# Performance work log

Measured on AMD Instinct MI355X. Metric: run time of the kernel, lower is better.

Reference implementation:

```python
import jax, jax.numpy as jnp
import numpy as np

B, L, D, H, FF = 2, 2048, 2048, 16, 8192
DH = D // H
NEG = -1e9


def setup_inputs() -> dict:
    key = jax.random.key(0)
    ks = jax.random.split(key, 9)
    x = jax.random.normal(ks[0], (B, L, D), dtype=jnp.float32)
    # additive causal mask, broadcastable to [B, H, L, L]
    causal = jnp.triu(jnp.full((L, L), NEG, dtype=jnp.float32), k=1)
    mask = causal[None, None, :, :]
    s = 1.0 / np.sqrt(D)
    Wq = jax.random.normal(ks[1], (D, D), dtype=jnp.float32) * s
    Wk = jax.random.normal(ks[2], (D, D), dtype=jnp.float32) * s
    Wv = jax.random.normal(ks[3], (D, D), dtype=jnp.float32) * s
    Wo = jax.random.normal(ks[4], (D, D), dtype=jnp.float32) * s
    W_up = jax.random.normal(ks[5], (FF, D), dtype=jnp.float32) * s
    b_up = jnp.zeros((FF,), dtype=jnp.float32)
    W_down = jax.random.normal(ks[6], (D, FF), dtype=jnp.float32) * (1.0 / np.sqrt(FF))
    return {"x": x, "mask": mask, "Wq": Wq, "Wk": Wk, "Wv": Wv, "Wo": Wo,
            "W_up": W_up, "b_up": b_up, "W_down": W_down}


def reference(x, mask, Wq, Wk, Wv, Wo, W_up, b_up, W_down):
    b, l, d = x.shape
    # projections (torch Linear: y = x @ W.T); reshape to [B, H, L, DH]
    q = (x @ Wq.T).reshape(b, l, H, DH).transpose(0, 2, 1, 3)
    k = (x @ Wk.T).reshape(b, l, H, DH).transpose(0, 2, 1, 3)
    v = (x @ Wv.T).reshape(b, l, H, DH).transpose(0, 2, 1, 3)
    # NOTE: original module applies NO 1/sqrt(d_head) scaling
    scores = jnp.einsum('bhqd,bhkd->bhqk', q, k) + mask
    attn = jax.nn.softmax(scores, axis=-1)
    out = jnp.einsum('bhqk,bhkd->bhqd', attn, v)
    out = out.transpose(0, 2, 1, 3).reshape(b, l, d)
    x = x + out @ Wo.T
    h = jax.nn.relu(x @ W_up.T + b_up)
    return x + h @ W_down.T
```

## Files before the change

### kernel.cpp

```cpp
#include <hip/hip_runtime.h>
#include <stdint.h>

typedef _Float16 f16;
typedef __attribute__((ext_vector_type(8))) _Float16 f16x8;
typedef __attribute__((ext_vector_type(4))) _Float16 f16x4;
typedef __attribute__((ext_vector_type(2))) __fp16 fp16x2;
typedef __attribute__((ext_vector_type(4))) float f32x4;
typedef __attribute__((ext_vector_type(16))) float f32x16;
typedef __attribute__((ext_vector_type(4))) unsigned u32x4;

__device__ __forceinline__ void gload16(void* lds, const void* gc) {
  void* g = const_cast<void*>(gc);
  __builtin_amdgcn_global_load_lds((__attribute__((address_space(1))) void*)g,
                                   (__attribute__((address_space(3))) void*)lds,
                                   16, 0, 0);
}

__device__ __forceinline__ unsigned pkrtz(float a, float b) {
  union { fp16x2 h; unsigned u; } c;
  c.h = __builtin_amdgcn_cvt_pkrtz(a, b);
  return c.u;
}

__global__ __launch_bounds__(256) void k_cast(const float* __restrict__ in,
                                              f16* __restrict__ out, int n4) {
  int stride = gridDim.x * blockDim.x;
  for (int i = blockIdx.x * blockDim.x + threadIdx.x; i < n4; i += stride) {
    float4 v = ((const float4*)in)[i];
    f16x4 o;
    o[0] = (f16)v.x; o[1] = (f16)v.y; o[2] = (f16)v.z; o[3] = (f16)v.w;
    ((f16x4*)out)[i] = o;
  }
}

__global__ __launch_bounds__(256) void k_cast4(const float* __restrict__ s0, const float* __restrict__ s1,
                                               const float* __restrict__ s2, const float* __restrict__ s3,
                                               f16* __restrict__ d0, f16* __restrict__ d1,
                                               f16* __restrict__ d2, f16* __restrict__ d3, int n4) {
  const int which = blockIdx.y;
  const float* in = which == 0 ? s0 : which == 1 ? s1 : which == 2 ? s2 : s3;
  f16* out = which == 0 ? d0 : which == 1 ? d1 : which == 2 ? d2 : d3;
  int stride = gridDim.x * blockDim.x;
  for (int i = blockIdx.x * blockDim.x + threadIdx.x; i < n4; i += stride) {
    float4 v = ((const float4*)in)[i];
    f16x4 o;
    o[0] = (f16)v.x; o[1] = (f16)v.y; o[2] = (f16)v.z; o[3] = (f16)v.w;
    ((f16x4*)out)[i] = o;
  }
}

__global__ __launch_bounds__(256) void k_cast2w(const float* __restrict__ s0, const float* __restrict__ s1,
                                                f16* __restrict__ d0, f16* __restrict__ d1, int n4) {
  const int which = blockIdx.y;
  const float* in = which == 0 ? s0 : s1;
  f16* out = which == 0 ? d0 : d1;
  int stride = gridDim.x * blockDim.x;
  for (int i = blockIdx.x * blockDim.x + threadIdx.x; i < n4; i += stride) {
    float4 v = ((const float4*)in)[i];
    f16x4 o;
    o[0] = (f16)v.x; o[1] = (f16)v.y; o[2] = (f16)v.z; o[3] = (f16)v.w;
    ((f16x4*)out)[i] = o;
  }
}

__global__ __launch_bounds__(256) void k_transpose_v(const f16* __restrict__ vp,
                                                     f16* __restrict__ vt) {
  __shared__ __attribute__((aligned(16))) f16 tile[64][66];
  const int lt = blockIdx.x, dt = blockIdx.y, bh = blockIdx.z;
  const int t = threadIdx.x;
  const int r = t >> 3, c = 8 * (t & 7);
  const f16* src = vp + ((size_t)bh * 2048 + lt * 64) * 128 + dt * 64;
#pragma unroll
  for (int i = 0; i < 2; ++i) {
    union { f16x8 v; unsigned u[4]; } uu;
    uu.v = *(const f16x8*)&src[(size_t)(i * 32 + r) * 128 + c];
#pragma unroll
    for (int j = 0; j < 4; ++j)
      *(unsigned*)&tile[i * 32 + r][c + 2 * j] = uu.u[j];
  }
  __syncthreads();
  f16* dst = vt + ((size_t)bh * 128 + dt * 64) * 2048 + lt * 64;
#pragma unroll
  for (int i = 0; i < 2; ++i) {
    const int dr = i * 32 + r;
    f16x8 o;
#pragma unroll
    for (int e = 0; e < 8; ++e) o[e] = tile[c + e][dr];
    *(f16x8*)&dst[(size_t)dr * 2048 + c] = o;
  }
}

__global__ __launch_bounds__(256) void k_fuseout(const f16* __restrict__ x1b,
                                                 const float* __restrict__ p0,
                                                 const float* __restrict__ p1,
                                                 float* __restrict__ out, int n4) {
  int stride = gridDim.x * blockDim.x;
  for (int i = blockIdx.x * blockDim.x + threadIdx.x; i < n4; i += stride) {
    float4 a = ((const float4*)p0)[i];
    float4 b = ((const float4*)p1)[i];
    f16x4 xb = ((const f16x4*)x1b)[i];
    float4 o;
    o.x = (float)xb[0] + a.x + b.x;
    o.y = (float)xb[1] + a.y + b.y;
    o.z = (float)xb[2] + a.z + b.z;
    o.w = (float)xb[3] + a.w + b.w;
    ((float4*)out)[i] = o;
  }
}

template <int EPI, int SPLITOUT, int BK>
__global__ __launch_bounds__(256, 4) void gemm_nt(const f16* __restrict__ A,
                                                  const f16* __restrict__ B,
                                                  int Kit, int ld, int N,
                                                  const float* __restrict__ res,
                                                  f16* __restrict__ outb) {
  constexpr int TSZ = 128 * BK;
  constexpr int CH  = 2048;
  constexpr int RPC = CH / BK;
  constexpr int NCH = 128 / RPC;
  constexpr int CW  = BK / 8;
  __shared__ __attribute__((aligned(16))) f16 As[TSZ];
  __shared__ __attribute__((aligned(16))) f16 Bs[TSZ];
  const int t = threadIdx.x;
  const int l = t & 63;
  const int w = t >> 6;
  const int wr = w >> 1, wc = w & 1;

  const int nwg = gridDim.x * gridDim.y;
  const int id = blockIdx.y * gridDim.x + blockIdx.x;
  const int sw = (id & 7) * (nwg >> 3) + (id >> 3);
  const int bn = sw % gridDim.x;
  const int bm = sw / gridDim.x;

  f32x4 acc[4][4] = {};

  const size_t aoff = (size_t)bm * 128 * ld;
  const size_t boff = (size_t)bn * 128 * ld;

  const int sr = t / CW;
  const int sc = 8 * (t % CW);
  const int lbase = w * 512;

  const int lr = l & 15, lq = l >> 4;
  const int nk = Kit / BK;
  for (int kt = 0; kt < nk; ++kt) {
    const size_t gbase = (size_t)kt * BK + (size_t)sr * ld + sc;
#pragma unroll
    for (int j = 0; j < NCH; ++j) {
      gload16(As + j * CH + lbase, A + aoff + (size_t)j * RPC * ld + gbase);
      gload16(Bs + j * CH + lbase, B + boff + (size_t)j * RPC * ld + gbase);
    }
    __syncthreads();
#pragma unroll
    for (int kk = 0; kk < BK / 32; ++kk) {
      f16x8 af[4], bfr[4];
#pragma unroll
      for (int m = 0; m < 4; ++m)
        af[m] = *(const f16x8*)&As[(wr * 64 + m * 16 + lr) * BK + kk * 32 + 8 * lq];
#pragma unroll
      for (int n = 0; n < 4; ++n)
        bfr[n] = *(const f16x8*)&Bs[(wc * 64 + n * 16 + lr) * BK + kk * 32 + 8 * lq];
#pragma unroll
      for (int m = 0; m < 4; ++m)
#pragma unroll
        for (int n = 0; n < 4; ++n)
          acc[m][n] = __builtin_amdgcn_mfma_f32_16x16x32_f16(af[m], bfr[n], acc[m][n], 0, 0, 0);
    }
    __syncthreads();
  }

#pragma unroll
  for (int m = 0; m < 4; ++m) {
#pragma unroll
    for (int r = 0; r < 4; ++r) {
      const int grow = bm * 128 + wr * 64 + m * 16 + lq * 4 + r;
#pragma unroll
      for (int n = 0; n < 4; ++n) {
        const int gcol = bn * 128 + wc * 64 + n * 16 + lr;
        const size_t idx = (size_t)grow * N + gcol;
        outb[idx] = (f16)(res[idx] + acc[m][n][r]);
      }
    }
  }
}

template <int EPI, int SPLITOUT>
__global__ __launch_bounds__(512, 2) void gemm8(const f16* __restrict__ A,
                                                const f16* __restrict__ B,
                                                int Kit, int ld, int N,
                                                const float* __restrict__ bias,
                                                float* __restrict__ outf,
                                                float* __restrict__ outf2,
                                                f16* __restrict__ outb,
                                                f16* __restrict__ outb_lo,
                                                f16* __restrict__ outv) {
  __shared__ __attribute__((aligned(16))) f16 As[4 * 8192];
  __shared__ __attribute__((aligned(16))) f16 Bs[4 * 8192];
  const int t = threadIdx.x;
  const int l = t & 63;
  const int w = t >> 6;
  const int wm = w >> 2, wn = w & 3;

  const int nwg = gridDim.x * gridDim.y;
  const int id = blockIdx.y * gridDim.x + blockIdx.x;
  const int sw = (id & 7) * (nwg >> 3) + (id >> 3);
  const int bn = sw % gridDim.x;
  const int bm = sw / gridDim.x;
  const int k0 = blockIdx.z * Kit;

  const size_t aoff = (size_t)(bm * 256) * ld + k0;
  const size_t boff = (size_t)(bn * 256) * ld + k0;

  const int r0 = t >> 2;
  const int gsw = (t & 3) ^ (r0 & 3) ^ ((r0 >> 2) & 3);
  const int ldsb = (t >> 6) * 512;

  auto stage = [&](int tt, int b) {
    const size_t col = (size_t)tt * 32 + gsw * 8;
#pragma unroll
    for (int j = 0; j < 2; ++j) {
      const size_t grow = (size_t)(j * 128 + r0) * ld + col;
      gload16(As + b * 8192 + j * 4096 + ldsb, A + aoff + grow);
      gload16(Bs + b * 8192 + j * 4096 + ldsb, B + boff + grow);
    }
  };

  f32x4 acc[8][4] = {};

  const int lr = l & 15, lq = l >> 4;
  const int xg = (lr & 3) ^ ((lr >> 2) & 3);
  const int nt = Kit >> 5;

  stage(0, 0);
  stage(1, 1);
  stage(2, 2);
  asm volatile("s_waitcnt vmcnt(8)" ::: "memory");
  __builtin_amdgcn_s_barrier();

  for (int kt = 0; kt < nt; ++kt) {
    const int b = kt & 3;
    const f16* Ab = As + b * 8192;
    const f16* Bb = Bs + b * 8192;
    f16x8 af[8], bf[4];
#pragma unroll
    for (int m = 0; m < 8; ++m) {
      const int row = wm * 128 + m * 16 + lr;
      af[m] = *(const f16x8*)&Ab[row * 32 + (lq ^ xg) * 8];
    }
#pragma unroll
    for (int n = 0; n < 4; ++n) {
      const int row = wn * 64 + n * 16 + lr;
      bf[n] = *(const f16x8*)&Bb[row * 32 + (lq ^ xg) * 8];
    }
    if (kt + 3 < nt) stage(kt + 3, (kt + 3) & 3);
    __builtin_amdgcn_s_setprio(1);
#pragma unroll
    for (int m = 0; m < 8; ++m)
#pragma unroll
      for (int n = 0; n < 4; ++n)
        acc[m][n] = __builtin_amdgcn_mfma_f32_16x16x32_f16(af[m], bf[n], acc[m][n], 0, 0, 0);
    __builtin_amdgcn_s_setprio(0);
    if (kt + 3 < nt) {
      asm volatile("s_waitcnt vmcnt(8)" ::: "memory");
    } else if (kt + 2 < nt) {
      asm volatile("s_waitcnt vmcnt(4)" ::: "memory");
    } else {
      asm volatile("s_waitcnt vmcnt(0)" ::: "memory");
    }
    __builtin_amdgcn_s_barrier();
  }

  const size_t QKS = (size_t)8 << 20;
#pragma unroll
  for (int m = 0; m < 8; ++m) {
#pragma unroll
    for (int r = 0; r < 4; ++r) {
      const int grow = bm * 256 + wm * 128 + m * 16 + lq * 4 + r;
#pragma unroll
      for (int n = 0; n < 4; ++n) {
        const int gcol = bn * 256 + wn * 64 + n * 16 + lr;
        const float v = acc[m][n][r];
        if constexpr (EPI == 0) {
          const int which = gcol >> 11;
          const int hcol = gcol & 2047;
          const int bb = grow >> 11, ll = grow & 2047;
          const int hh = hcol >> 7, dh = hcol & 127;
          const size_t idx = ((size_t)((bb * 16 + hh) * 2048 + ll) << 7) + dh;
          const f16 hv = (f16)v;
          if (which == 2) {
            outv[idx] = hv;
          } else {
            outb[which * QKS + idx] = hv;
            if constexpr (SPLITOUT) outb_lo[which * QKS + idx] = (f16)(v - (float)hv);
          }
        } else if constexpr (EPI == 2) {
          const size_t idx = (size_t)grow * N + gcol;
          outb[idx] = (f16)fmaxf(v + bias[gcol], 0.f);
        } else {
          const size_t idx = (size_t)grow * N + gcol;
          (blockIdx.z ? outf2 : outf)[idx] = v;
        }
      }
    }
  }
}

__global__ __launch_bounds__(256) void k_attn(const f16* __restrict__ q_hi,
                                              const f16* __restrict__ q_lo,
                                              const f16* __restrict__ k_hi,
                                              const f16* __restrict__ k_lo,
                                              const f16* __restrict__ vtp,
                                              f16* __restrict__ op) {
  __shared__ __attribute__((aligned(16))) f16 Ks_hi[64 * 128];
  __shared__ __attribute__((aligned(16))) f16 Ks_lo[64 * 128];
  __shared__ __attribute__((aligned(16))) f16 Vs[128 * 64];
  const int t = threadIdx.x, l = t & 63, w = t >> 6;
  const int flat = (int)blockIdx.x;
  const int s_ = flat >> 5;
  const int bh = flat & 31;
  const int qb = (s_ < 8) ? (15 - s_) : (s_ - 8);
  const int q0 = qb * 128;
  const int lh = l >> 5, lm = l & 31;
  const int wrow0 = q0 + 32 * w;
  const int myrow = wrow0 + lm;

  const f16* qhp = q_hi + (size_t)bh * 2048 * 128;
  const f16* qlp = q_lo + (size_t)bh * 2048 * 128;
  const f16* khp = k_hi + (size_t)bh * 2048 * 128;
  const f16* klp = k_lo + (size_t)bh * 2048 * 128;
  const f16* vhp = vtp + (size_t)bh * 128 * 2048;

  const int krow = t >> 4, kg = t & 15;
  const int vrow = t >> 3, vg = t & 7;

  f16x8 aqh[8], aql[8];
#pragma unroll
  for (int c = 0; c < 8; ++c) {
    const size_t qi = (size_t)myrow * 128 + c * 16 + 8 * lh;
    aqh[c] = *(const f16x8*)&qhp[qi];
    aql[c] = *(const f16x8*)&qlp[qi];
  }

  f32x16 acc[4] = {};
  float mr = -1e30f, sr = 0.f;

  const int ntile = 2 * qb + 2;
  for (int kt = 0; kt < ntile; ++kt) {
    f16x8 tkh[4], tkl[4], tv[4];
#pragma unroll
    for (int i = 0; i < 4; ++i) {
      const size_t ki = (size_t)(kt * 64 + i * 16 + krow) * 128 + 8 * kg;
      tkh[i] = *(const f16x8*)&khp[ki];
      tkl[i] = *(const f16x8*)&klp[ki];
      tv[i] = *(const f16x8*)&vhp[(size_t)(i * 32 + vrow) * 2048 + kt * 64 + 8 * vg];
    }
    __syncthreads();
#pragma unroll
    for (int i = 0; i < 4; ++i) {
      const int kr = i * 16 + krow;
      const int g = kg ^ (kr & 7);
      *(f16x8*)&Ks_hi[kr * 128 + 8 * g] = tkh[i];
      *(f16x8*)&Ks_lo[kr * 128 + 8 * g] = tkl[i];
      const int vr = i * 32 + vrow;
      const int gv = vg ^ (vr & 7);
      *(f16x8*)&Vs[vr * 64 + 8 * gv] = tv[i];
    }
    __syncthreads();

    if (kt * 64 >= wrow0 + 32) continue;

    f32x16 s0, s1;
    __builtin_amdgcn_s_setprio(1);
    {
      f32x16 zh = {}, zl = {};
#pragma unroll
      for (int c = 0; c < 8; ++c) {
        const int g = (2 * c + lh) ^ (lm & 7);
        const f16x8 bh_ = *(const f16x8*)&Ks_hi[lm * 128 + 8 * g];
        const f16x8 bl_ = *(const f16x8*)&Ks_lo[lm * 128 + 8 * g];
        zh = __builtin_amdgcn_mfma_f32_32x32x16_f16(bh_, aqh[c], zh, 0, 0, 0);
        zl = __builtin_amdgcn_mfma_f32_32x32x16_f16(bh_, aql[c], zl, 0, 0, 0);
        zl = __builtin_amdgcn_mfma_f32_32x32x16_f16(bl_, aqh[c], zl, 0, 0, 0);
      }
      s0 = zh + zl;
    }
    {
      f32x16 zh = {}, zl = {};
#pragma unroll
      for (int c = 0; c < 8; ++c) {
        const int g = (2 * c + lh) ^ (lm & 7);
        const f16x8 bh_ = *(const f16x8*)&Ks_hi[(32 + lm) * 128 + 8 * g];
        const f16x8 bl_ = *(const f16x8*)&Ks_lo[(32 + lm) * 128 + 8 * g];
        zh = __builtin_amdgcn_mfma_f32_32x32x16_f16(bh_, aqh[c], zh, 0, 0, 0);
        zl = __builtin_amdgcn_mfma_f32_32x32x16_f16(bh_, aql[c], zl, 0, 0, 0);
        zl = __builtin_amdgcn_mfma_f32_32x32x16_f16(bl_, aqh[c], zl, 0, 0, 0);
      }
      s1 = zh + zl;
    }
    __builtin_amdgcn_s_setprio(0);

    if (kt * 64 + 63 > wrow0) {
#pragma unroll
      for (int j = 0; j < 16; ++j) {
        const int keyl = (j & 3) + 8 * (j >> 2) + 4 * lh;
        if (kt * 64 + keyl > myrow) s0[j] = -1e30f;
        if (kt * 64 + 32 + keyl > myrow) s1[j] = -1e30f;
      }
    }

    float m = -1e30f;
#pragma unroll
    for (int j = 0; j < 16; ++j) m = fmaxf(m, fmaxf(s0[j], s1[j]));
    m = fmaxf(m, __shfl_xor(m, 32));
    if (__any(m > mr + 8.f)) {
      const float mnew = fmaxf(mr, m);
      const float sc = __expf(mr - mnew);
      mr = mnew;
      sr *= sc;
#pragma unroll
      for (int j = 0; j < 16; ++j) {
        const float scj = __shfl(sc, (j & 3) + 8 * (j >> 2) + 4 * lh);
#pragma unroll
        for (int ct = 0; ct < 4; ++ct) acc[ct][j] *= scj;
      }
    }
    float p0v[16], p1v[16];
    float ts = 0.f;
#pragma unroll
    for (int j = 0; j < 16; ++j) {
      p0v[j] = __expf(s0[j] - mr);
      p1v[j] = __expf(s1[j] - mr);
      ts += p0v[j] + p1v[j];
    }
    sr += ts + __shfl_xor(ts, 32);

    unsigned u[16];
#pragma unroll
    for (int m2 = 0; m2 < 8; ++m2) {
      u[m2] = pkrtz(p0v[2 * m2], p0v[2 * m2 + 1]);
      u[8 + m2] = pkrtz(p1v[2 * m2], p1v[2 * m2 + 1]);
    }
    unsigned ys[8];
#pragma unroll
    for (int m2 = 0; m2 < 8; ++m2) {
      const int q_ = m2 >> 1, h_ = m2 & 1;
      const unsigned xs = lh ? u[4 * q_ + h_] : u[4 * q_ + 2 + h_];
      ys[m2] = __shfl_xor(xs, 32);
    }
    f16x8 pf[4];
#pragma unroll
    for (int kk = 0; kk < 4; ++kk) {
      union { u32x4 u4; f16x8 h8; } cv;
      if (lh == 0) {
        cv.u4[0] = u[4 * kk];     cv.u4[1] = u[4 * kk + 1];
        cv.u4[2] = ys[2 * kk];    cv.u4[3] = ys[2 * kk + 1];
      } else {
        cv.u4[0] = ys[2 * kk];    cv.u4[1] = ys[2 * kk + 1];
        cv.u4[2] = u[4 * kk + 2]; cv.u4[3] = u[4 * kk + 3];
      }
      pf[kk] = cv.h8;
    }

    __builtin_amdgcn_s_setprio(1);
#pragma unroll
    for (int ct = 0; ct < 4; ++ct) {
      const int dcol = ct * 32 + lm;
#pragma unroll
      for (int kk = 0; kk < 4; ++kk) {
        const int gv = (2 * kk + lh) ^ (dcol & 7);
        const f16x8 bv = *(const f16x8*)&Vs[dcol * 64 + 8 * gv];
        acc[ct] = __builtin_amdgcn_mfma_f32_32x32x16_f16(pf[kk], bv, acc[ct], 0, 0, 0);
      }
    }
    __builtin_amdgcn_s_setprio(0);
  }

  const int bb = bh >> 4, hh = bh & 15;
  const float inv = 1.f / sr;
#pragma unroll
  for (int j = 0; j < 16; ++j) {
    const int rl = (j & 3) + 8 * (j >> 2) + 4 * lh;
    const float invj = __shfl(inv, rl);
    const size_t row = (size_t)(bb * 2048 + wrow0 + rl);
#pragma unroll
    for (int ct = 0; ct < 4; ++ct)
      op[row * 2048 + hh * 128 + ct * 32 + lm] = (f16)(acc[ct][j] * invj);
  }
}

extern "C" void kernel_launch(void* const* d_in, const int* in_sizes, int n_in,
                              void* d_out, int out_size, void* d_ws, size_t ws_size,
                              hipStream_t stream) {
  const float* x   = (const float*)d_in[0];
  const float* Wq  = (const float*)d_in[2];
  const float* Wk  = (const float*)d_in[3];
  const float* Wv  = (const float*)d_in[4];
  const float* Wo  = (const float*)d_in[5];
  const float* Wup = (const float*)d_in[6];
  const float* bup = (const float*)d_in[7];
  const float* Wdn = (const float*)d_in[8];
  float* out = (float*)d_out;

  const size_t M1 = 1u << 20;
  f16* W = (f16*)d_ws;
  f16* x_hi    = W + 0 * M1;
  f16* wqkv_hi = W + 8 * M1;
  f16* wo_hi   = W + 20 * M1;
  f16* wup_hi  = W + 24 * M1;
  f16* wdn_hi  = W + 40 * M1;
  f16* q_hi    = W + 56 * M1;
  f16* q_lo    = W + 72 * M1;
  f16* vp      = W + 88 * M1;
  f16* vtb     = W + 96 * M1;
  f16* x1b   = x_hi;
  float* p0  = (float*)(W + 24 * M1);
  f16* hb    = W + 56 * M1;
  float* p1  = (float*)(W + 88 * M1);
  f16* attno = vp;
  if (ws_size < (size_t)104 * M1 * sizeof(f16)) return;

  auto cg = [](size_t n4) { size_t g = (n4 + 255) / 256; return (unsigned)(g > 2048 ? 2048 : g); };
  dim3 b256(256);
  dim3 b512(512);
  k_cast<<<cg(2 * M1), b256, 0, stream>>>(x, x_hi, (int)(2 * M1));
  k_cast4<<<dim3(cg(1 * M1), 4), b256, 0, stream>>>(
      Wq, Wk, Wv, Wo,
      wqkv_hi, wqkv_hi + 4 * M1, wqkv_hi + 8 * M1, wo_hi, (int)(1 * M1));
  k_cast2w<<<dim3(cg(4 * M1), 2), b256, 0, stream>>>(
      Wup, Wdn, wup_hi, wdn_hi, (int)(4 * M1));

  gemm8<0, 1><<<dim3(24, 16), b512, 0, stream>>>(
      x_hi, wqkv_hi, 2048, 2048, 6144,
      nullptr, nullptr, nullptr, q_hi, q_lo, vp);
  k_transpose_v<<<dim3(32, 2, 32), b256, 0, stream>>>(vp, vtb);
  k_attn<<<dim3(512), b256, 0, stream>>>(
      q_hi, q_lo, q_hi + 8 * M1, q_lo + 8 * M1, vtb, attno);
  gemm_nt<1, 0, 64><<<dim3(16, 32), b256, 0, stream>>>(
      attno, wo_hi, 2048, 2048, 2048, x, x1b);
  gemm8<2, 0><<<dim3(32, 16), b512, 0, stream>>>(
      x1b, wup_hi, 2048, 2048, 8192,
      bup, nullptr, nullptr, hb, nullptr, nullptr);
  gemm8<3, 0><<<dim3(8, 16, 2), b512, 0, stream>>>(
      hb, wdn_hi, 4096, 8192, 2048,
      nullptr, p0, p1, nullptr, nullptr, nullptr);
  k_fuseout<<<2048, b256, 0, stream>>>(x1b, p0, p1, out, (int)(2 * M1));
}
```

Before: 710.5 us.

## Shrink gemm8 tile to 128x256 with 3-stage buffer and raise occupancy

The main GEMM kernel's M tile is halved from 256 to 128 rows, and its LDS ring drops from 4 stages to 3. This cuts accumulator registers and shared memory so launch bounds can ask for 4 workgroups per CU, and the grids double in the M dimension to match. The attention kernel now stages each K/V tile in two halves to lower register pressure and requests 3 blocks per CU. The trade-off is less B-tile reuse per block, a shallower prefetch, and more global traffic for the weight operand.

```diff
diff --git a/kernel.cpp b/kernel.cpp
--- a/kernel.cpp
+++ b/kernel.cpp
@@ -185,7 +185,7 @@
 }
 
 template <int EPI, int SPLITOUT>
-__global__ __launch_bounds__(512, 2) void gemm8(const f16* __restrict__ A,
+__global__ __launch_bounds__(512, 4) void gemm8(const f16* __restrict__ A,
                                                 const f16* __restrict__ B,
                                                 int Kit, int ld, int N,
                                                 const float* __restrict__ bias,
@@ -194,8 +194,8 @@
                                                 f16* __restrict__ outb,
                                                 f16* __restrict__ outb_lo,
                                                 f16* __restrict__ outv) {
-  __shared__ __attribute__((aligned(16))) f16 As[4 * 8192];
-  __shared__ __attribute__((aligned(16))) f16 Bs[4 * 8192];
+  __shared__ __attribute__((aligned(16))) f16 As[3 * 4096];
+  __shared__ __attribute__((aligned(16))) f16 Bs[3 * 8192];
   const int t = threadIdx.x;
   const int l = t & 63;
   const int w = t >> 6;
@@ -208,7 +208,7 @@
   const int bm = sw / gridDim.x;
   const int k0 = blockIdx.z * Kit;
 
-  const size_t aoff = (size_t)(bm * 256) * ld + k0;
+  const size_t aoff = (size_t)(bm * 128) * ld + k0;
   const size_t boff = (size_t)(bn * 256) * ld + k0;
 
   const int r0 = t >> 2;
@@ -217,15 +217,13 @@
 
   auto stage = [&](int tt, int b) {
     const size_t col = (size_t)tt * 32 + gsw * 8;
-#pragma unroll
-    for (int j = 0; j < 2; ++j) {
-      const size_t grow = (size_t)(j * 128 + r0) * ld + col;
-      gload16(As + b * 8192 + j * 4096 + ldsb, A + aoff + grow);
-      gload16(Bs + b * 8192 + j * 4096 + ldsb, B + boff + grow);
-    }
+    gload16(As + b * 4096 + ldsb, A + aoff + (size_t)r0 * ld + col);
+#pragma unroll
+    for (int j = 0; j < 2; ++j)
+      gload16(Bs + b * 8192 + j * 4096 + ldsb, B + boff + (size_t)(j * 128 + r0) * ld + col);
   };
 
-  f32x4 acc[8][4] = {};
+  f32x4 acc[4][4] = {};
 
   const int lr = l & 15, lq = l >> 4;
   const int xg = (lr & 3) ^ ((lr >> 2) & 3);
@@ -233,37 +231,30 @@
 
   stage(0, 0);
   stage(1, 1);
-  stage(2, 2);
-  asm volatile("s_waitcnt vmcnt(8)" ::: "memory");
+  asm volatile("s_waitcnt vmcnt(3)" ::: "memory");
   __builtin_amdgcn_s_barrier();
 
   for (int kt = 0; kt < nt; ++kt) {
-    const int b = kt & 3;
-    const f16* Ab = As + b * 8192;
+    const int b = kt % 3;
+    const f16* Ab = As + b * 4096;
     const f16* Bb = Bs + b * 8192;
-    f16x8 af[8], bf[4];
-#pragma unroll
-    for (int m = 0; m < 8; ++m) {
-      const int row = wm * 128 + m * 16 + lr;
-      af[m] = *(const f16x8*)&Ab[row * 32 + (lq ^ xg) * 8];
-    }
-#pragma unroll
-    for (int n = 0; n < 4; ++n) {
-      const int row = wn * 64 + n * 16 + lr;
-      bf[n] = *(const f16x8*)&Bb[row * 32 + (lq ^ xg) * 8];
-    }
-    if (kt + 3 < nt) stage(kt + 3, (kt + 3) & 3);
+    f16x8 af[4], bf[4];
+#pragma unroll
+    for (int m = 0; m < 4; ++m)
+      af[m] = *(const f16x8*)&Ab[(wm * 64 + m * 16 + lr) * 32 + ((lq ^ xg)) * 8];
+#pragma unroll
+    for (int n = 0; n < 4; ++n)
+      bf[n] = *(const f16x8*)&Bb[(wn * 64 + n * 16 + lr) * 32 + ((lq ^ xg)) * 8];
+    if (kt + 2 < nt) stage(kt + 2, (kt + 2) % 3);
     __builtin_amdgcn_s_setprio(1);
 #pragma unroll
-    for (int m = 0; m < 8; ++m)
+    for (int m = 0; m < 4; ++m)
 #pragma unroll
       for (int n = 0; n < 4; ++n)
         acc[m][n] = __builtin_amdgcn_mfma_f32_16x16x32_f16(af[m], bf[n], acc[m][n], 0, 0, 0);
     __builtin_amdgcn_s_setprio(0);
-    if (kt + 3 < nt) {
-      asm volatile("s_waitcnt vmcnt(8)" ::: "memory");
-    } else if (kt + 2 < nt) {
-      asm volatile("s_waitcnt vmcnt(4)" ::: "memory");
+    if (kt + 2 < nt) {
+      asm volatile("s_waitcnt vmcnt(3)" ::: "memory");
     } else {
       asm volatile("s_waitcnt vmcnt(0)" ::: "memory");
     }
@@ -272,10 +263,10 @@
 
   const size_t QKS = (size_t)8 << 20;
 #pragma unroll
-  for (int m = 0; m < 8; ++m) {
+  for (int m = 0; m < 4; ++m) {
 #pragma unroll
     for (int r = 0; r < 4; ++r) {
-      const int grow = bm * 256 + wm * 128 + m * 16 + lq * 4 + r;
+      const int grow = bm * 128 + wm * 64 + m * 16 + lq * 4 + r;
 #pragma unroll
       for (int n = 0; n < 4; ++n) {
         const int gcol = bn * 256 + wn * 64 + n * 16 + lr;
@@ -305,12 +296,12 @@
   }
 }
 
-__global__ __launch_bounds__(256) void k_attn(const f16* __restrict__ q_hi,
-                                              const f16* __restrict__ q_lo,
-                                              const f16* __restrict__ k_hi,
-                                              const f16* __restrict__ k_lo,
-                                              const f16* __restrict__ vtp,
-                                              f16* __restrict__ op) {
+__global__ __launch_bounds__(256, 3) void k_attn(const f16* __restrict__ q_hi,
+                                                 const f16* __restrict__ q_lo,
+                                                 const f16* __restrict__ k_hi,
+                                                 const f16* __restrict__ k_lo,
+                                                 const f16* __restrict__ vtp,
+                                                 f16* __restrict__ op) {
   __shared__ __attribute__((aligned(16))) f16 Ks_hi[64 * 128];
   __shared__ __attribute__((aligned(16))) f16 Ks_lo[64 * 128];
   __shared__ __attribute__((aligned(16))) f16 Vs[128 * 64];
@@ -346,24 +337,41 @@
 
   const int ntile = 2 * qb + 2;
   for (int kt = 0; kt < ntile; ++kt) {
-    f16x8 tkh[4], tkl[4], tv[4];
-#pragma unroll
-    for (int i = 0; i < 4; ++i) {
+    f16x8 kh2[2], kl2[2], v2[2];
+#pragma unroll
+    for (int i = 0; i < 2; ++i) {
       const size_t ki = (size_t)(kt * 64 + i * 16 + krow) * 128 + 8 * kg;
-      tkh[i] = *(const f16x8*)&khp[ki];
-      tkl[i] = *(const f16x8*)&klp[ki];
-      tv[i] = *(const f16x8*)&vhp[(size_t)(i * 32 + vrow) * 2048 + kt * 64 + 8 * vg];
+      kh2[i] = *(const f16x8*)&khp[ki];
+      kl2[i] = *(const f16x8*)&klp[ki];
+      v2[i] = *(const f16x8*)&vhp[(size_t)(i * 32 + vrow) * 2048 + kt * 64 + 8 * vg];
     }
     __syncthreads();
 #pragma unroll
-    for (int i = 0; i < 4; ++i) {
+    for (int i = 0; i < 2; ++i) {
       const int kr = i * 16 + krow;
       const int g = kg ^ (kr & 7);
-      *(f16x8*)&Ks_hi[kr * 128 + 8 * g] = tkh[i];
-      *(f16x8*)&Ks_lo[kr * 128 + 8 * g] = tkl[i];
+      *(f16x8*)&Ks_hi[kr * 128 + 8 * g] = kh2[i];
+      *(f16x8*)&Ks_lo[kr * 128 + 8 * g] = kl2[i];
       const int vr = i * 32 + vrow;
       const int gv = vg ^ (vr & 7);
-      *(f16x8*)&Vs[vr * 64 + 8 * gv] = tv[i];
+      *(f16x8*)&Vs[vr * 64 + 8 * gv] = v2[i];
+    }
+#pragma unroll
+    for (int i = 0; i < 2; ++i) {
+      const size_t ki = (size_t)(kt * 64 + (i + 2) * 16 + krow) * 128 + 8 * kg;
+      kh2[i] = *(const f16x8*)&khp[ki];
+      kl2[i] = *(const f16x8*)&klp[ki];
+      v2[i] = *(const f16x8*)&vhp[(size_t)((i + 2) * 32 + vrow) * 2048 + kt * 64 + 8 * vg];
+    }
+#pragma unroll
+    for (int i = 0; i < 2; ++i) {
+      const int kr = (i + 2) * 16 + krow;
+      const int g = kg ^ (kr & 7);
+      *(f16x8*)&Ks_hi[kr * 128 + 8 * g] = kh2[i];
+      *(f16x8*)&Ks_lo[kr * 128 + 8 * g] = kl2[i];
+      const int vr = (i + 2) * 32 + vrow;
+      const int gv = vg ^ (vr & 7);
+      *(f16x8*)&Vs[vr * 64 + 8 * gv] = v2[i];
     }
     __syncthreads();
 
@@ -529,7 +537,7 @@
   k_cast2w<<<dim3(cg(4 * M1), 2), b256, 0, stream>>>(
       Wup, Wdn, wup_hi, wdn_hi, (int)(4 * M1));
 
-  gemm8<0, 1><<<dim3(24, 16), b512, 0, stream>>>(
+  gemm8<0, 1><<<dim3(24, 32), b512, 0, stream>>>(
       x_hi, wqkv_hi, 2048, 2048, 6144,
       nullptr, nullptr, nullptr, q_hi, q_lo, vp);
   k_transpose_v<<<dim3(32, 2, 32), b256, 0, stream>>>(vp, vtb);
@@ -537,10 +545,10 @@
       q_hi, q_lo, q_hi + 8 * M1, q_lo + 8 * M1, vtb, attno);
   gemm_nt<1, 0, 64><<<dim3(16, 32), b256, 0, stream>>>(
       attno, wo_hi, 2048, 2048, 2048, x, x1b);
-  gemm8<2, 0><<<dim3(32, 16), b512, 0, stream>>>(
+  gemm8<2, 0><<<dim3(32, 32), b512, 0, stream>>>(
       x1b, wup_hi, 2048, 2048, 8192,
       bup, nullptr, nullptr, hb, nullptr, nullptr);
-  gemm8<3, 0><<<dim3(8, 16, 2), b512, 0, stream>>>(
+  gemm8<3, 0><<<dim3(8, 32, 2), b512, 0, stream>>>(
       hb, wdn_hi, 4096, 8192, 2048,
       nullptr, p0, p1, nullptr, nullptr, nullptr);
   k_fuseout<<<2048, b256, 0, stream>>>(x1b, p0, p1, out, (int)(2 * M1));
```

Result: slower. 998.0 us (+40.5%).
